# Optimization experiments

Measured on AMD Instinct MI355X. Metric: run time of the kernel, lower is better.

## Reference

```python
import jax, jax.numpy as jnp
import numpy as np

IN_NC = 32
OUT_NC = 32
HIDDEN = 192  # in_nc * expand_ratio(6)
KS = 3
EPS = 1e-5


def setup_inputs() -> dict:
    key = jax.random.key(0)
    k1, k2 = jax.random.split(key)
    b, h, w = 8, 128, 128
    fh = fw = 8
    hyper = IN_NC * HIDDEN + HIDDEN * KS * KS + HIDDEN * OUT_NC  # 14016
    return {
        "x": jax.random.normal(k1, (b, IN_NC, h, w), jnp.float32),
        "s": jax.random.normal(k2, (b, hyper, fh, fw), jnp.float32),
        "g1": jnp.ones((HIDDEN,), jnp.float32),
        "b1": jnp.zeros((HIDDEN,), jnp.float32),
        "g2": jnp.ones((HIDDEN,), jnp.float32),
        "b2": jnp.zeros((HIDDEN,), jnp.float32),
        "g3": jnp.ones((OUT_NC,), jnp.float32),
        "b3": jnp.zeros((OUT_NC,), jnp.float32),
    }


def _bn(x, gamma, beta):
    # x: [P, H, W, C]; training-mode BatchNorm2d over (P, H, W) per channel
    mean = jnp.mean(x, axis=(0, 1, 2))
    var = jnp.var(x, axis=(0, 1, 2))  # biased, matches torch normalization
    return (x - mean) * jax.lax.rsqrt(var + EPS) * gamma + beta


def _relu6(x):
    return jnp.clip(x, 0.0, 6.0)


def _forward(x, s, g1, b1, g2, b2, g3, b3):
    b, c, h, w = x.shape
    fh, fw = s.shape[-2], s.shape[-1]
    ph, pw = h // fh, w // fw
    kh, kw = ph + 2, pw + 2  # padding (1,1)

    # reflect-pad then unfold into per-patch tiles [P, kh, kw, c]
    xp = jnp.pad(x, ((0, 0), (0, 0), (1, 1), (1, 1)), mode="reflect")
    xp = xp.transpose(0, 2, 3, 1)  # [b, h+2, w+2, c]
    ih = jnp.arange(fh)[:, None] * ph + jnp.arange(kh)[None, :]  # [fh, kh]
    iw = jnp.arange(fw)[:, None] * pw + jnp.arange(kw)[None, :]  # [fw, kw]
    t = xp[:, ih]            # [b, fh, kh, w+2, c]
    t = t[:, :, :, iw]       # [b, fh, kh, fw, kw, c]
    patches = t.transpose(0, 1, 3, 2, 4, 5).reshape(b * fh * fw, kh, kw, c)

    # per-patch hypernet weights
    wt = s.transpose(0, 2, 3, 1).reshape(b * fh * fw, -1)  # [P, hyper]
    r1 = IN_NC * HIDDEN
    r2 = r1 + HIDDEN * KS * KS
    w1 = wt[:, :r1].reshape(-1, HIDDEN, IN_NC)          # pointwise expand
    w2 = wt[:, r1:r2].reshape(-1, HIDDEN, KS, KS)        # depthwise 3x3
    w3 = wt[:, r2:].reshape(-1, OUT_NC, HIDDEN)          # pointwise project

    # 1x1 expand + BN + ReLU6
    x1 = jnp.einsum("pijc,poc->pijo", patches, w1)       # [P, kh, kw, hidden]
    x1 = _relu6(_bn(x1, g1, b1))

    # depthwise 3x3 (valid, stride 1) + BN + ReLU6
    ii = jnp.arange(ph)[:, None] + jnp.arange(KS)[None, :]
    jj = jnp.arange(pw)[:, None] + jnp.arange(KS)[None, :]
    win = x1[:, ii]          # [P, ph, 3, kw, hidden]
    win = win[:, :, :, jj]   # [P, ph, 3, pw, 3, hidden]
    x2 = jnp.einsum("piujvc,pcuv->pijc", win, w2)        # [P, ph, pw, hidden]
    x2 = _relu6(_bn(x2, g2, b2))

    # 1x1 project + BN
    x3 = jnp.einsum("pijc,poc->pijo", x2, w3)            # [P, ph, pw, out]
    x3 = _bn(x3, g3, b3)

    out = x3.reshape(b, fh, fw, ph, pw, OUT_NC)
    out = out.transpose(0, 5, 1, 3, 2, 4).reshape(b, OUT_NC, h, w)
    return x + out  # use_res_connect: stride==1 and in_nc==out_nc


def reference(x, s, g1, b1, g2, b2, g3, b3):
    return _forward(x, s, g1, b1, g2, b2, g3, b3)
```

## Files before the change

kernel.cpp:

```cpp
#include <hip/hip_runtime.h>

#define EPS 1e-5f

namespace {
constexpr int HYPER = 14016;
constexpr int HID   = 192;
constexpr int A1    = 324;
constexpr int A2    = 256;
constexpr int P_TOT = 512;
constexpr int W1SZ  = 6144;
constexpr int WT2SZ = 7872;
constexpr int R3OFF = 1728;

constexpr size_t WB1_B = 0;
constexpr size_t WT2_B = 6291456;
constexpr size_t X2_B  = WT2_B + 16121856;
constexpr size_t X3_B  = X2_B + 50331648;
constexpr size_t SUM_B = X3_B + 8388608;
}

typedef __attribute__((ext_vector_type(8))) short bf16x8;
typedef __attribute__((ext_vector_type(4))) float f32x4;

__device__ __forceinline__ float relu6f(float v) { return fminf(fmaxf(v, 0.f), 6.f); }

__device__ __forceinline__ float bf2f(unsigned int h) {
  return __uint_as_float(h << 16);
}
__device__ __forceinline__ unsigned short f2bf(float f) {
  unsigned int u = __float_as_uint(f);
  return (unsigned short)((u + 0x7FFFu + ((u >> 16) & 1u)) >> 16);
}

__device__ __host__ __forceinline__ int afrag_slot(int o, int c) {
  return (o >> 4) * 512 + (c >> 3) * 128 + (o & 15) * 8 + (c & 7);
}

__global__ __launch_bounds__(256) void k0_transpose(const float* __restrict__ s,
                                                    unsigned short* __restrict__ wb1,
                                                    float* __restrict__ wt2) {
  __shared__ float tile[64][65];
  const int blk = blockIdx.x;
  const int b  = blk / 219;
  const int kt = blk - b * 219;
  const int k0 = kt * 64;
  const int t  = threadIdx.x;
  {
    const int f  = t & 63;
    const int kr = t >> 6;
    const float* sp = s + ((size_t)b * HYPER + k0 + kr) * 64 + f;
#pragma unroll
    for (int kk = 0; kk < 16; kk++)
      tile[kr + kk * 4][f] = sp[(size_t)kk * 4 * 64];
  }
  __syncthreads();
  {
    const int kk = t & 63;
    const int fr = t >> 6;
    if (kt < 96) {
      const int k = k0 + kk;
      const int o = k >> 5, c = k & 31;
      const int slot = afrag_slot(o, c);
      unsigned short* wp = wb1 + ((size_t)b * 64 + fr) * W1SZ + slot;
#pragma unroll
      for (int ff = 0; ff < 16; ff++)
        wp[(size_t)ff * 4 * W1SZ] = f2bf(tile[kk][fr + ff * 4]);
    } else {
      float* wp = wt2 + ((size_t)b * 64 + fr) * WT2SZ + (k0 - W1SZ) + kk;
#pragma unroll
      for (int ff = 0; ff < 16; ff++)
        wp[(size_t)ff * 4 * WT2SZ] = tile[kk][fr + ff * 4];
    }
  }
}

__global__ __launch_bounds__(256) void k1_stats(const float* __restrict__ x,
                                                const unsigned short* __restrict__ wb1,
                                                float* __restrict__ sums) {
  __shared__ __align__(16) unsigned short pL[21 * 512];
  __shared__ float stat[384];
  const int p  = blockIdx.x;
  const int b  = p >> 6;
  const int fi = (p >> 3) & 7;
  const int fj = p & 7;
  const int t  = threadIdx.x;

  for (int i = t; i < 384; i += 256) stat[i] = 0.f;

  const int row0 = fi * 16 - 1, col0 = fj * 16 - 1;
  const float* xb = x + (size_t)b * 32 * 128 * 128;
  for (int idx = t; idx < 32 * A1; idx += 256) {
    int c  = idx / A1;
    int ij = idx - c * A1;
    int ii = ij / 18;
    int jj = ij - ii * 18;
    int r  = row0 + ii; r  = (r  < 0) ? 1 : (r  > 127) ? 126 : r;
    int cl = col0 + jj; cl = (cl < 0) ? 1 : (cl > 127) ? 126 : cl;
    int slot = ((ij >> 4) * 4 + (c >> 3)) * 128 + (ij & 15) * 8 + (c & 7);
    pL[slot] = f2bf(xb[((size_t)c * 128 + r) * 128 + cl]);
  }
  __syncthreads();

  const int lane = t & 63;
  const int wv   = t >> 6;
  const int m16  = lane & 15;
  const int quad = lane >> 4;
  const unsigned short* wbp = wb1 + (size_t)p * W1SZ;

  for (int oi = 0; oi < 3; oi++) {
    const int ot = wv + oi * 4;
    bf16x8 a = *(const bf16x8*)(wbp + ot * 512 + lane * 8);
    float sacc[4] = {0.f, 0.f, 0.f, 0.f};
    float qacc[4] = {0.f, 0.f, 0.f, 0.f};
    for (int jt = 0; jt < 21; jt++) {
      bf16x8 bb = *(const bf16x8*)&pL[jt * 512 + lane * 8];
      f32x4 d = __builtin_amdgcn_mfma_f32_16x16x32_bf16(a, bb, (f32x4){0.f, 0.f, 0.f, 0.f}, 0, 0, 0);
      const int ij = jt * 16 + m16;
      if (ij < A1) {
#pragma unroll
        for (int r = 0; r < 4; r++) {
          float v = d[r];
          sacc[r] += v;
          qacc[r] = fmaf(v, v, qacc[r]);
        }
      }
    }
#pragma unroll
    for (int r = 0; r < 4; r++) {
      float sv = sacc[r], qv = qacc[r];
#pragma unroll
      for (int msk = 1; msk < 16; msk <<= 1) {
        sv += __shfl_xor(sv, msk, 64);
        qv += __shfl_xor(qv, msk, 64);
      }
      if (m16 == 0) {
        int o = ot * 16 + quad * 4 + r;
        atomicAdd(&stat[o], sv);
        atomicAdd(&stat[192 + o], qv);
      }
    }
  }
  __syncthreads();
  for (int i = t; i < 384; i += 256) atomicAdd(&sums[i], stat[i]);
}

__global__ __launch_bounds__(256) void k2_fused(const float* __restrict__ x,
                                                const unsigned short* __restrict__ wb1,
                                                const float* __restrict__ wt2,
                                                const float* __restrict__ sums,
                                                const float* __restrict__ g1,
                                                const float* __restrict__ b1,
                                                unsigned short* __restrict__ x2,
                                                float* __restrict__ sums2) {
  __shared__ __align__(16) unsigned short pL[21 * 512];
  __shared__ __align__(16) unsigned short xc[16 * 328];
  __shared__ __align__(16) unsigned short x2s[256 * 18];
  __shared__ float w2L[HID * 9];
  __shared__ float sc[HID], sh[HID];
  __shared__ float st2[384];
  const int p  = blockIdx.x;
  const int b  = p >> 6;
  const int fi = (p >> 3) & 7;
  const int fj = p & 7;
  const int t  = threadIdx.x;

  const float inv1 = 1.f / 165888.f;
  for (int c = t; c < HID; c += 256) {
    float m   = sums[c] * inv1;
    float var = sums[192 + c] * inv1 - m * m;
    float scl = g1[c] * rsqrtf(var + EPS);
    sc[c] = scl;
    sh[c] = b1[c] - m * scl;
  }
  for (int i = t; i < 384; i += 256) st2[i] = 0.f;
  {
    const float* wtp = wt2 + (size_t)p * WT2SZ;
    for (int i = t; i < HID * 9; i += 256) w2L[i] = wtp[i];
  }

  const int row0 = fi * 16 - 1, col0 = fj * 16 - 1;
  const float* xb = x + (size_t)b * 32 * 128 * 128;
  for (int idx = t; idx < 32 * A1; idx += 256) {
    int c  = idx / A1;
    int ij = idx - c * A1;
    int ii = ij / 18;
    int jj = ij - ii * 18;
    int r  = row0 + ii; r  = (r  < 0) ? 1 : (r  > 127) ? 126 : r;
    int cl = col0 + jj; cl = (cl < 0) ? 1 : (cl > 127) ? 126 : cl;
    int slot = ((ij >> 4) * 4 + (c >> 3)) * 128 + (ij & 15) * 8 + (c & 7);
    pL[slot] = f2bf(xb[((size_t)c * 128 + r) * 128 + cl]);
  }
  __syncthreads();

  const int lane = t & 63;
  const int wv   = t >> 6;
  const int m16  = lane & 15;
  const int quad = lane >> 4;
  const int ih  = t >> 7;
  const int cdw = (t >> 3) & 15;
  const int jp  = t & 7;
  const unsigned short* wbp = wb1 + (size_t)p * W1SZ;
  unsigned short* x2base = x2 + (size_t)p * 12 * 4096;

  auto conv1 = [&](int rt) {
    bf16x8 a = *(const bf16x8*)(wbp + rt * 512 + lane * 8);
    for (int jt = wv; jt < 21; jt += 4) {
      bf16x8 bb = *(const bf16x8*)&pL[jt * 512 + lane * 8];
      f32x4 d = __builtin_amdgcn_mfma_f32_16x16x32_bf16(a, bb, (f32x4){0.f, 0.f, 0.f, 0.f}, 0, 0, 0);
      const int ij = jt * 16 + m16;
      if (ij < A1) {
#pragma unroll
        for (int r = 0; r < 4; r++) {
          int cl = quad * 4 + r;
          int ch = rt * 16 + cl;
          float v = relu6f(fmaf(d[r], sc[ch], sh[ch]));
          xc[cl * 328 + ij] = f2bf(v);
        }
      }
    }
  };

  conv1(0);
  __syncthreads();

  for (int rt = 0; rt < 12; rt++) {
    {
      const int ch = rt * 16 + cdw;
      float wr[9];
#pragma unroll
      for (int u = 0; u < 9; u++) wr[u] = w2L[ch * 9 + u];
      float a0[8], a1[8];
#pragma unroll
      for (int i = 0; i < 8; i++) { a0[i] = 0.f; a1[i] = 0.f; }
      const unsigned short* xcc = &xc[cdw * 328];
#pragma unroll
      for (int rr = 0; rr < 10; rr++) {
        const int rg = ih * 8 + rr;
        unsigned int d0 = *(const unsigned int*)&xcc[rg * 18 + jp * 2];
        unsigned int d1 = *(const unsigned int*)&xcc[rg * 18 + jp * 2 + 2];
        float v0 = bf2f(d0 & 0xFFFFu), v1 = bf2f(d0 >> 16);
        float v2 = bf2f(d1 & 0xFFFFu), v3 = bf2f(d1 >> 16);
#pragma unroll
        for (int u = 0; u < 3; u++) {
          int il = rr - u;
          if (il >= 0 && il < 8) {
            a0[il] = fmaf(v0, wr[u * 3 + 0], fmaf(v1, wr[u * 3 + 1], fmaf(v2, wr[u * 3 + 2], a0[il])));
            a1[il] = fmaf(v1, wr[u * 3 + 0], fmaf(v2, wr[u * 3 + 1], fmaf(v3, wr[u * 3 + 2], a1[il])));
          }
        }
      }
      float ls = 0.f, lq = 0.f;
#pragma unroll
      for (int il = 0; il < 8; il++) {
        const int ig = ih * 8 + il;
        const int j0 = jp * 2;
        unsigned short h0 = f2bf(a0[il]);
        unsigned short h1 = f2bf(a1[il]);
        float r0 = bf2f(h0), r1 = bf2f(h1);
        ls += r0 + r1;
        lq = fmaf(r0, r0, fmaf(r1, r1, lq));
        x2s[(ig * 16 + j0) * 18 + cdw]     = h0;
        x2s[(ig * 16 + j0 + 1) * 18 + cdw] = h1;
      }
      ls += __shfl_xor(ls, 1, 64); lq += __shfl_xor(lq, 1, 64);
      ls += __shfl_xor(ls, 2, 64); lq += __shfl_xor(lq, 2, 64);
      ls += __shfl_xor(ls, 4, 64); lq += __shfl_xor(lq, 4, 64);
      if (jp == 0) {
        atomicAdd(&st2[ch], ls);
        atomicAdd(&st2[192 + ch], lq);
      }
    }
    __syncthreads();
    {
      unsigned short* dst = x2base + (size_t)rt * 4096;
#pragma unroll
      for (int k = 0; k < 4; k++) {
        int g  = (k * 256 + t) * 4;
        int ij = g >> 4, c0 = g & 15;
        unsigned int v0 = *(const unsigned int*)&x2s[ij * 18 + c0];
        unsigned int v1 = *(const unsigned int*)&x2s[ij * 18 + c0 + 2];
        uint2 v; v.x = v0; v.y = v1;
        *(uint2*)&dst[g] = v;
      }
    }
    if (rt < 11) conv1(rt + 1);
    __syncthreads();
  }
  for (int i = t; i < 384; i += 256) atomicAdd(&sums2[i], st2[i]);
}

__global__ __launch_bounds__(256) void k3_pw2(const unsigned short* __restrict__ x2,
                                              const float* __restrict__ wt2,
                                              const float* __restrict__ sums2,
                                              const float* __restrict__ g2,
                                              const float* __restrict__ b2,
                                              unsigned short* __restrict__ x3,
                                              float* __restrict__ sums3) {
  __shared__ __align__(16) unsigned short wA[12 * 512];
  __shared__ float sc[HID], sh[HID];
  __shared__ float st3[64];
  const int blk  = blockIdx.x;
  const int p    = blk >> 1;
  const int half = blk & 1;
  const int t    = threadIdx.x;
  const float inv = 1.f / 131072.f;
  for (int c = t; c < HID; c += 256) {
    float m   = sums2[c] * inv;
    float var = sums2[192 + c] * inv - m * m;
    float scl = g2[c] * rsqrtf(var + EPS);
    sc[c] = scl;
    sh[c] = b2[c] - m * scl;
  }
  if (t < 64) st3[t] = 0.f;
  const float* w3p = wt2 + (size_t)p * WT2SZ + R3OFF;
  for (int idx = t; idx < 32 * 48; idx += 256) {
    int o  = idx / 48;
    int c4 = idx - o * 48;
    float4 v = *(const float4*)&w3p[o * HID + c4 * 4];
    int slot = ((o >> 4) * 6 + (c4 >> 3)) * 512 + ((((c4 >> 1) & 3) * 16) + (o & 15)) * 8 + (c4 & 1) * 4;
    ushort4 u;
    u.x = f2bf(v.x); u.y = f2bf(v.y); u.z = f2bf(v.z); u.w = f2bf(v.w);
    *(ushort4*)&wA[slot] = u;
  }
  __syncthreads();
  const int lane = t & 63;
  const int wv   = t >> 6;
  const int m16  = lane & 15;
  const int kg   = lane >> 4;
  bf16x8 aF[2][6];
#pragma unroll
  for (int ot = 0; ot < 2; ot++)
#pragma unroll
    for (int ks = 0; ks < 6; ks++)
      aF[ot][ks] = *(const bf16x8*)&wA[(ot * 6 + ks) * 512 + lane * 8];
  const unsigned short* x2p = x2 + (size_t)p * 12 * 4096;
  f32x4 acc[2][2];
#pragma unroll
  for (int it = 0; it < 2; it++)
#pragma unroll
    for (int ot = 0; ot < 2; ot++)
#pragma unroll
      for (int r = 0; r < 4; r++) acc[it][ot][r] = 0.f;
#pragma unroll
  for (int it = 0; it < 2; it++) {
    const int ijt = half * 8 + wv + it * 4;
    const int ij  = ijt * 16 + m16;
    const unsigned short* brow = x2p + (size_t)(kg >> 1) * 4096 + (size_t)ij * 16 + (kg & 1) * 8;
#pragma unroll
    for (int ks = 0; ks < 6; ks++) {
      ushort4 u0 = *(const ushort4*)&brow[ks * 8192];
      ushort4 u1 = *(const ushort4*)&brow[ks * 8192 + 4];
      const float* scp = &sc[ks * 32 + kg * 8];
      const float* shp = &sh[ks * 32 + kg * 8];
      unsigned short uu[8] = {u0.x, u0.y, u0.z, u0.w, u1.x, u1.y, u1.z, u1.w};
      bf16x8 bb;
#pragma unroll
      for (int j = 0; j < 8; j++) {
        float y = relu6f(fmaf(bf2f(uu[j]), scp[j], shp[j]));
        bb[j] = (short)f2bf(y);
      }
      acc[it][0] = __builtin_amdgcn_mfma_f32_16x16x32_bf16(aF[0][ks], bb, acc[it][0], 0, 0, 0);
      acc[it][1] = __builtin_amdgcn_mfma_f32_16x16x32_bf16(aF[1][ks], bb, acc[it][1], 0, 0, 0);
    }
  }
  unsigned short* x3p = x3 + (size_t)p * 32 * A2;
  float sacc[2][4] = {{0.f}}, qacc[2][4] = {{0.f}};
#pragma unroll
  for (int it = 0; it < 2; it++) {
    const int ijt = half * 8 + wv + it * 4;
#pragma unroll
    for (int ot = 0; ot < 2; ot++) {
#pragma unroll
      for (int r = 0; r < 4; r++) {
        unsigned short h = f2bf(acc[it][ot][r]);
        float v = bf2f(h);
        x3p[(size_t)(ot * 16 + kg * 4 + r) * A2 + ijt * 16 + m16] = h;
        sacc[ot][r] += v;
        qacc[ot][r] = fmaf(v, v, qacc[ot][r]);
      }
    }
  }
#pragma unroll
  for (int ot = 0; ot < 2; ot++)
#pragma unroll
    for (int r = 0; r < 4; r++) {
      float sv = sacc[ot][r], qv = qacc[ot][r];
#pragma unroll
      for (int msk = 1; msk < 16; msk <<= 1) {
        sv += __shfl_xor(sv, msk, 64);
        qv += __shfl_xor(qv, msk, 64);
      }
      if (m16 == 0) {
        int o = ot * 16 + kg * 4 + r;
        atomicAdd(&st3[o], sv);
        atomicAdd(&st3[32 + o], qv);
      }
    }
  __syncthreads();
  if (t < 64) atomicAdd(&sums3[t], st3[t]);
}

__global__ __launch_bounds__(256) void k4_out(const float* __restrict__ x,
                                              const unsigned short* __restrict__ x3,
                                              const float* __restrict__ sums3,
                                              const float* __restrict__ g3,
                                              const float* __restrict__ b3,
                                              float* __restrict__ out) {
  const int idx4 = blockIdx.x * 256 + threadIdx.x;
  const int w4 = idx4 & 31;
  int tmp = idx4 >> 5;
  const int h = tmp & 127; tmp >>= 7;
  const int o = tmp & 31;
  const int b = tmp >> 5;
  const int fi = h >> 4, i = h & 15;
  const int fj = w4 >> 2;
  const int j0 = (w4 & 3) * 4;
  const int p   = b * 64 + fi * 8 + fj;
  const int ij0 = i * 16 + j0;
  const float inv = 1.f / 131072.f;
  float m   = sums3[o] * inv;
  float var = sums3[32 + o] * inv - m * m;
  float sv  = g3[o] * rsqrtf(var + EPS);
  float shv = b3[o] - m * sv;
  float4 xv = *(const float4*)&x[(size_t)idx4 * 4];
  ushort4 u = *(const ushort4*)&x3[((size_t)p * 32 + o) * A2 + ij0];
  float4 r;
  r.x = fmaf(bf2f(u.x), sv, shv) + xv.x;
  r.y = fmaf(bf2f(u.y), sv, shv) + xv.y;
  r.z = fmaf(bf2f(u.z), sv, shv) + xv.z;
  r.w = fmaf(bf2f(u.w), sv, shv) + xv.w;
  *(float4*)&out[(size_t)idx4 * 4] = r;
}

extern "C" void kernel_launch(void* const* d_in, const int* in_sizes, int n_in,
                              void* d_out, int out_size, void* d_ws, size_t ws_size,
                              hipStream_t stream) {
  const float* x  = (const float*)d_in[0];
  const float* s  = (const float*)d_in[1];
  const float* g1 = (const float*)d_in[2];
  const float* b1 = (const float*)d_in[3];
  const float* g2 = (const float*)d_in[4];
  const float* b2 = (const float*)d_in[5];
  const float* g3 = (const float*)d_in[6];
  const float* b3 = (const float*)d_in[7];
  char* base = (char*)d_ws;
  unsigned short* wb1  = (unsigned short*)(base + WB1_B);
  float*          wt2  = (float*)(base + WT2_B);
  unsigned short* x2   = (unsigned short*)(base + X2_B);
  unsigned short* x3   = (unsigned short*)(base + X3_B);
  float*          sums = (float*)(base + SUM_B);
  float* out = (float*)d_out;

  hipMemsetAsync(sums, 0, 832 * sizeof(float), stream);
  k0_transpose<<<8 * 219, 256, 0, stream>>>(s, wb1, wt2);
  k1_stats<<<P_TOT, 256, 0, stream>>>(x, wb1, sums);
  k2_fused<<<P_TOT, 256, 0, stream>>>(x, wb1, wt2, sums, g1, b1, x2, sums + 384);
  k3_pw2<<<1024, 256, 0, stream>>>(x2, wt2, sums + 384, g2, b2, x3, sums + 768);
  k4_out<<<4096, 256, 0, stream>>>(x, x3, sums + 768, g3, b3, out);
}
```

Measured before the change: 223.0 us.

## Split fused depthwise kernel into two half-patch blocks per patch

New measurement: 228.7 us. +2.6%, slower.

```diff
diff --git a/kernel.cpp b/kernel.cpp
--- a/kernel.cpp
+++ b/kernel.cpp
@@ -152,13 +152,18 @@
                                                 const float* __restrict__ b1,
                                                 unsigned short* __restrict__ x2,
                                                 float* __restrict__ sums2) {
-  __shared__ __align__(16) unsigned short pL[21 * 512];
-  __shared__ __align__(16) unsigned short xc[16 * 328];
-  __shared__ __align__(16) unsigned short x2s[256 * 18];
+  constexpr int NIJ = 180;
+  constexpr int NT  = 12;
+  constexpr int XCP = 184;
+  __shared__ __align__(16) unsigned short pL[NT * 512];
+  __shared__ __align__(16) unsigned short xc[16 * XCP];
+  __shared__ __align__(16) unsigned short x2s[128 * 18];
   __shared__ float w2L[HID * 9];
   __shared__ float sc[HID], sh[HID];
   __shared__ float st2[384];
-  const int p  = blockIdx.x;
+  const int blk = blockIdx.x;
+  const int p  = blk >> 1;
+  const int hh = blk & 1;
   const int b  = p >> 6;
   const int fi = (p >> 3) & 7;
   const int fj = p & 7;
@@ -178,11 +183,11 @@
     for (int i = t; i < HID * 9; i += 256) w2L[i] = wtp[i];
   }
 
-  const int row0 = fi * 16 - 1, col0 = fj * 16 - 1;
+  const int row0 = fi * 16 - 1 + hh * 8, col0 = fj * 16 - 1;
   const float* xb = x + (size_t)b * 32 * 128 * 128;
-  for (int idx = t; idx < 32 * A1; idx += 256) {
-    int c  = idx / A1;
-    int ij = idx - c * A1;
+  for (int idx = t; idx < 32 * NIJ; idx += 256) {
+    int c  = idx / NIJ;
+    int ij = idx - c * NIJ;
     int ii = ij / 18;
     int jj = ij - ii * 18;
     int r  = row0 + ii; r  = (r  < 0) ? 1 : (r  > 127) ? 126 : r;
@@ -196,25 +201,25 @@
   const int wv   = t >> 6;
   const int m16  = lane & 15;
   const int quad = lane >> 4;
-  const int ih  = t >> 7;
+  const int i2  = t >> 7;
   const int cdw = (t >> 3) & 15;
   const int jp  = t & 7;
   const unsigned short* wbp = wb1 + (size_t)p * W1SZ;
-  unsigned short* x2base = x2 + (size_t)p * 12 * 4096;
+  unsigned short* x2base = x2 + (size_t)p * 12 * 4096 + (size_t)hh * 2048;
 
   auto conv1 = [&](int rt) {
     bf16x8 a = *(const bf16x8*)(wbp + rt * 512 + lane * 8);
-    for (int jt = wv; jt < 21; jt += 4) {
+    for (int jt = wv; jt < NT; jt += 4) {
       bf16x8 bb = *(const bf16x8*)&pL[jt * 512 + lane * 8];
       f32x4 d = __builtin_amdgcn_mfma_f32_16x16x32_bf16(a, bb, (f32x4){0.f, 0.f, 0.f, 0.f}, 0, 0, 0);
       const int ij = jt * 16 + m16;
-      if (ij < A1) {
+      if (ij < NIJ) {
 #pragma unroll
         for (int r = 0; r < 4; r++) {
           int cl = quad * 4 + r;
           int ch = rt * 16 + cl;
           float v = relu6f(fmaf(d[r], sc[ch], sh[ch]));
-          xc[cl * 328 + ij] = f2bf(v);
+          xc[cl * XCP + ij] = f2bf(v);
         }
       }
     }
@@ -229,13 +234,13 @@
       float wr[9];
 #pragma unroll
       for (int u = 0; u < 9; u++) wr[u] = w2L[ch * 9 + u];
-      float a0[8], a1[8];
-#pragma unroll
-      for (int i = 0; i < 8; i++) { a0[i] = 0.f; a1[i] = 0.f; }
-      const unsigned short* xcc = &xc[cdw * 328];
-#pragma unroll
-      for (int rr = 0; rr < 10; rr++) {
-        const int rg = ih * 8 + rr;
+      float a0[4], a1[4];
+#pragma unroll
+      for (int i = 0; i < 4; i++) { a0[i] = 0.f; a1[i] = 0.f; }
+      const unsigned short* xcc = &xc[cdw * XCP];
+#pragma unroll
+      for (int rr = 0; rr < 6; rr++) {
+        const int rg = i2 * 4 + rr;
         unsigned int d0 = *(const unsigned int*)&xcc[rg * 18 + jp * 2];
         unsigned int d1 = *(const unsigned int*)&xcc[rg * 18 + jp * 2 + 2];
         float v0 = bf2f(d0 & 0xFFFFu), v1 = bf2f(d0 >> 16);
@@ -243,7 +248,7 @@
 #pragma unroll
         for (int u = 0; u < 3; u++) {
           int il = rr - u;
-          if (il >= 0 && il < 8) {
+          if (il >= 0 && il < 4) {
             a0[il] = fmaf(v0, wr[u * 3 + 0], fmaf(v1, wr[u * 3 + 1], fmaf(v2, wr[u * 3 + 2], a0[il])));
             a1[il] = fmaf(v1, wr[u * 3 + 0], fmaf(v2, wr[u * 3 + 1], fmaf(v3, wr[u * 3 + 2], a1[il])));
           }
@@ -251,8 +256,8 @@
       }
       float ls = 0.f, lq = 0.f;
 #pragma unroll
-      for (int il = 0; il < 8; il++) {
-        const int ig = ih * 8 + il;
+      for (int il = 0; il < 4; il++) {
+        const int ig = i2 * 4 + il;
         const int j0 = jp * 2;
         unsigned short h0 = f2bf(a0[il]);
         unsigned short h1 = f2bf(a1[il]);
@@ -274,7 +279,7 @@
     {
       unsigned short* dst = x2base + (size_t)rt * 4096;
 #pragma unroll
-      for (int k = 0; k < 4; k++) {
+      for (int k = 0; k < 2; k++) {
         int g  = (k * 256 + t) * 4;
         int ij = g >> 4, c0 = g & 15;
         unsigned int v0 = *(const unsigned int*)&x2s[ij * 18 + c0];
@@ -454,7 +459,7 @@
   hipMemsetAsync(sums, 0, 832 * sizeof(float), stream);
   k0_transpose<<<8 * 219, 256, 0, stream>>>(s, wb1, wt2);
   k1_stats<<<P_TOT, 256, 0, stream>>>(x, wb1, sums);
-  k2_fused<<<P_TOT, 256, 0, stream>>>(x, wb1, wt2, sums, g1, b1, x2, sums + 384);
+  k2_fused<<<P_TOT * 2, 256, 0, stream>>>(x, wb1, wt2, sums, g1, b1, x2, sums + 384);
   k3_pw2<<<1024, 256, 0, stream>>>(x2, wt2, sums + 384, g2, b2, x3, sums + 768);
   k4_out<<<4096, 256, 0, stream>>>(x, x3, sums + 768, g3, b3, out);
 }
```

## Double k2 block size to 512 threads and use packed bf16 conversion instructions

Applied to the files above, without the earlier changes.

New measurement: 213.7 us. -4.2%, faster.

```diff
diff --git a/kernel.cpp b/kernel.cpp
--- a/kernel.cpp
+++ b/kernel.cpp
@@ -21,6 +21,7 @@
 
 typedef __attribute__((ext_vector_type(8))) short bf16x8;
 typedef __attribute__((ext_vector_type(4))) float f32x4;
+typedef __attribute__((ext_vector_type(4))) unsigned int u32x4;
 
 __device__ __forceinline__ float relu6f(float v) { return fminf(fmaxf(v, 0.f), 6.f); }
 
@@ -144,14 +145,14 @@
   for (int i = t; i < 384; i += 256) atomicAdd(&sums[i], stat[i]);
 }
 
-__global__ __launch_bounds__(256) void k2_fused(const float* __restrict__ x,
-                                                const unsigned short* __restrict__ wb1,
-                                                const float* __restrict__ wt2,
-                                                const float* __restrict__ sums,
-                                                const float* __restrict__ g1,
-                                                const float* __restrict__ b1,
-                                                unsigned short* __restrict__ x2,
-                                                float* __restrict__ sums2) {
+__global__ __launch_bounds__(512, 4) void k2_fused(const float* __restrict__ x,
+                                                   const unsigned short* __restrict__ wb1,
+                                                   const float* __restrict__ wt2,
+                                                   const float* __restrict__ sums,
+                                                   const float* __restrict__ g1,
+                                                   const float* __restrict__ b1,
+                                                   unsigned short* __restrict__ x2,
+                                                   float* __restrict__ sums2) {
   __shared__ __align__(16) unsigned short pL[21 * 512];
   __shared__ __align__(16) unsigned short xc[16 * 328];
   __shared__ __align__(16) unsigned short x2s[256 * 18];
@@ -165,22 +166,22 @@
   const int t  = threadIdx.x;
 
   const float inv1 = 1.f / 165888.f;
-  for (int c = t; c < HID; c += 256) {
-    float m   = sums[c] * inv1;
-    float var = sums[192 + c] * inv1 - m * m;
-    float scl = g1[c] * rsqrtf(var + EPS);
-    sc[c] = scl;
-    sh[c] = b1[c] - m * scl;
-  }
-  for (int i = t; i < 384; i += 256) st2[i] = 0.f;
+  if (t < HID) {
+    float m   = sums[t] * inv1;
+    float var = sums[192 + t] * inv1 - m * m;
+    float scl = g1[t] * rsqrtf(var + EPS);
+    sc[t] = scl;
+    sh[t] = b1[t] - m * scl;
+  }
+  if (t < 384) st2[t] = 0.f;
   {
     const float* wtp = wt2 + (size_t)p * WT2SZ;
-    for (int i = t; i < HID * 9; i += 256) w2L[i] = wtp[i];
+    for (int i = t; i < HID * 9; i += 512) w2L[i] = wtp[i];
   }
 
   const int row0 = fi * 16 - 1, col0 = fj * 16 - 1;
   const float* xb = x + (size_t)b * 32 * 128 * 128;
-  for (int idx = t; idx < 32 * A1; idx += 256) {
+  for (int idx = t; idx < 32 * A1; idx += 512) {
     int c  = idx / A1;
     int ij = idx - c * A1;
     int ii = ij / 18;
@@ -196,25 +197,31 @@
   const int wv   = t >> 6;
   const int m16  = lane & 15;
   const int quad = lane >> 4;
-  const int ih  = t >> 7;
+  const int ihq = t >> 7;
   const int cdw = (t >> 3) & 15;
   const int jp  = t & 7;
   const unsigned short* wbp = wb1 + (size_t)p * W1SZ;
-  unsigned short* x2base = x2 + (size_t)p * 12 * 4096;
+  unsigned short* x2base = x2 + (size_t)p * 49152;
 
   auto conv1 = [&](int rt) {
     bf16x8 a = *(const bf16x8*)(wbp + rt * 512 + lane * 8);
-    for (int jt = wv; jt < 21; jt += 4) {
+    float scv[4], shv[4];
+#pragma unroll
+    for (int r = 0; r < 4; r++) {
+      scv[r] = sc[rt * 16 + quad * 4 + r];
+      shv[r] = sh[rt * 16 + quad * 4 + r];
+    }
+    for (int jt = wv; jt < 21; jt += 8) {
       bf16x8 bb = *(const bf16x8*)&pL[jt * 512 + lane * 8];
       f32x4 d = __builtin_amdgcn_mfma_f32_16x16x32_bf16(a, bb, (f32x4){0.f, 0.f, 0.f, 0.f}, 0, 0, 0);
       const int ij = jt * 16 + m16;
       if (ij < A1) {
 #pragma unroll
         for (int r = 0; r < 4; r++) {
-          int cl = quad * 4 + r;
-          int ch = rt * 16 + cl;
-          float v = relu6f(fmaf(d[r], sc[ch], sh[ch]));
-          xc[cl * 328 + ij] = f2bf(v);
+          float v = relu6f(fmaf(d[r], scv[r], shv[r]));
+          unsigned int u;
+          asm("v_cvt_pk_bf16_f32 %0, %1, %2" : "=v"(u) : "v"(v), "v"(v));
+          xc[(quad * 4 + r) * 328 + ij] = (unsigned short)u;
         }
       }
     }
@@ -229,13 +236,13 @@
       float wr[9];
 #pragma unroll
       for (int u = 0; u < 9; u++) wr[u] = w2L[ch * 9 + u];
-      float a0[8], a1[8];
-#pragma unroll
-      for (int i = 0; i < 8; i++) { a0[i] = 0.f; a1[i] = 0.f; }
+      float a0[4], a1[4];
+#pragma unroll
+      for (int i = 0; i < 4; i++) { a0[i] = 0.f; a1[i] = 0.f; }
       const unsigned short* xcc = &xc[cdw * 328];
 #pragma unroll
-      for (int rr = 0; rr < 10; rr++) {
-        const int rg = ih * 8 + rr;
+      for (int rr = 0; rr < 6; rr++) {
+        const int rg = ihq * 4 + rr;
         unsigned int d0 = *(const unsigned int*)&xcc[rg * 18 + jp * 2];
         unsigned int d1 = *(const unsigned int*)&xcc[rg * 18 + jp * 2 + 2];
         float v0 = bf2f(d0 & 0xFFFFu), v1 = bf2f(d0 >> 16);
@@ -243,7 +250,7 @@
 #pragma unroll
         for (int u = 0; u < 3; u++) {
           int il = rr - u;
-          if (il >= 0 && il < 8) {
+          if (il >= 0 && il < 4) {
             a0[il] = fmaf(v0, wr[u * 3 + 0], fmaf(v1, wr[u * 3 + 1], fmaf(v2, wr[u * 3 + 2], a0[il])));
             a1[il] = fmaf(v1, wr[u * 3 + 0], fmaf(v2, wr[u * 3 + 1], fmaf(v3, wr[u * 3 + 2], a1[il])));
           }
@@ -251,16 +258,17 @@
       }
       float ls = 0.f, lq = 0.f;
 #pragma unroll
-      for (int il = 0; il < 8; il++) {
-        const int ig = ih * 8 + il;
+      for (int il = 0; il < 4; il++) {
+        const int ig = ihq * 4 + il;
         const int j0 = jp * 2;
-        unsigned short h0 = f2bf(a0[il]);
-        unsigned short h1 = f2bf(a1[il]);
-        float r0 = bf2f(h0), r1 = bf2f(h1);
-        ls += r0 + r1;
-        lq = fmaf(r0, r0, fmaf(r1, r1, lq));
-        x2s[(ig * 16 + j0) * 18 + cdw]     = h0;
-        x2s[(ig * 16 + j0 + 1) * 18 + cdw] = h1;
+        unsigned int ua;
+        asm("v_cvt_pk_bf16_f32 %0, %1, %2" : "=v"(ua) : "v"(a0[il]), "v"(a1[il]));
+        float s0 = __uint_as_float(ua << 16);
+        float s1 = __uint_as_float(ua & 0xFFFF0000u);
+        ls += s0 + s1;
+        lq = fmaf(s0, s0, fmaf(s1, s1, lq));
+        x2s[(ig * 16 + j0) * 18 + cdw]     = (unsigned short)ua;
+        x2s[(ig * 16 + j0 + 1) * 18 + cdw] = (unsigned short)(ua >> 16);
       }
       ls += __shfl_xor(ls, 1, 64); lq += __shfl_xor(lq, 1, 64);
       ls += __shfl_xor(ls, 2, 64); lq += __shfl_xor(lq, 2, 64);
@@ -274,8 +282,8 @@
     {
       unsigned short* dst = x2base + (size_t)rt * 4096;
 #pragma unroll
-      for (int k = 0; k < 4; k++) {
-        int g  = (k * 256 + t) * 4;
+      for (int k = 0; k < 2; k++) {
+        int g  = (k * 512 + t) * 4;
         int ij = g >> 4, c0 = g & 15;
         unsigned int v0 = *(const unsigned int*)&x2s[ij * 18 + c0];
         unsigned int v1 = *(const unsigned int*)&x2s[ij * 18 + c0 + 2];
@@ -286,7 +294,7 @@
     if (rt < 11) conv1(rt + 1);
     __syncthreads();
   }
-  for (int i = t; i < 384; i += 256) atomicAdd(&sums2[i], st2[i]);
+  for (int i = t; i < 384; i += 512) atomicAdd(&sums2[i], st2[i]);
 }
 
 __global__ __launch_bounds__(256) void k3_pw2(const unsigned short* __restrict__ x2,
@@ -348,17 +356,19 @@
     const unsigned short* brow = x2p + (size_t)(kg >> 1) * 4096 + (size_t)ij * 16 + (kg & 1) * 8;
 #pragma unroll
     for (int ks = 0; ks < 6; ks++) {
-      ushort4 u0 = *(const ushort4*)&brow[ks * 8192];
-      ushort4 u1 = *(const ushort4*)&brow[ks * 8192 + 4];
+      u32x4 uv = *(const u32x4*)&brow[ks * 8192];
       const float* scp = &sc[ks * 32 + kg * 8];
       const float* shp = &sh[ks * 32 + kg * 8];
-      unsigned short uu[8] = {u0.x, u0.y, u0.z, u0.w, u1.x, u1.y, u1.z, u1.w};
-      bf16x8 bb;
-#pragma unroll
-      for (int j = 0; j < 8; j++) {
-        float y = relu6f(fmaf(bf2f(uu[j]), scp[j], shp[j]));
-        bb[j] = (short)f2bf(y);
-      }
+      u32x4 pk;
+#pragma unroll
+      for (int q = 0; q < 4; q++) {
+        float ylo = relu6f(fmaf(__uint_as_float(uv[q] << 16),          scp[2 * q],     shp[2 * q]));
+        float yhi = relu6f(fmaf(__uint_as_float(uv[q] & 0xFFFF0000u),  scp[2 * q + 1], shp[2 * q + 1]));
+        unsigned int r;
+        asm("v_cvt_pk_bf16_f32 %0, %1, %2" : "=v"(r) : "v"(ylo), "v"(yhi));
+        pk[q] = r;
+      }
+      bf16x8 bb = __builtin_bit_cast(bf16x8, pk);
       acc[it][0] = __builtin_amdgcn_mfma_f32_16x16x32_bf16(aF[0][ks], bb, acc[it][0], 0, 0, 0);
       acc[it][1] = __builtin_amdgcn_mfma_f32_16x16x32_bf16(aF[1][ks], bb, acc[it][1], 0, 0, 0);
     }
@@ -371,12 +381,18 @@
 #pragma unroll
     for (int ot = 0; ot < 2; ot++) {
 #pragma unroll
-      for (int r = 0; r < 4; r++) {
-        unsigned short h = f2bf(acc[it][ot][r]);
-        float v = bf2f(h);
-        x3p[(size_t)(ot * 16 + kg * 4 + r) * A2 + ijt * 16 + m16] = h;
-        sacc[ot][r] += v;
-        qacc[ot][r] = fmaf(v, v, qacc[ot][r]);
+      for (int rp = 0; rp < 2; rp++) {
+        unsigned int ua;
+        asm("v_cvt_pk_bf16_f32 %0, %1, %2" : "=v"(ua)
+            : "v"(acc[it][ot][2 * rp]), "v"(acc[it][ot][2 * rp + 1]));
+        float v0 = __uint_as_float(ua << 16);
+        float v1 = __uint_as_float(ua & 0xFFFF0000u);
+        x3p[(size_t)(ot * 16 + kg * 4 + 2 * rp) * A2 + ijt * 16 + m16]     = (unsigned short)ua;
+        x3p[(size_t)(ot * 16 + kg * 4 + 2 * rp + 1) * A2 + ijt * 16 + m16] = (unsigned short)(ua >> 16);
+        sacc[ot][2 * rp]     += v0;
+        sacc[ot][2 * rp + 1] += v1;
+        qacc[ot][2 * rp]      = fmaf(v0, v0, qacc[ot][2 * rp]);
+        qacc[ot][2 * rp + 1]  = fmaf(v1, v1, qacc[ot][2 * rp + 1]);
       }
     }
   }
@@ -454,7 +470,7 @@
   hipMemsetAsync(sums, 0, 832 * sizeof(float), stream);
   k0_transpose<<<8 * 219, 256, 0, stream>>>(s, wb1, wt2);
   k1_stats<<<P_TOT, 256, 0, stream>>>(x, wb1, sums);
-  k2_fused<<<P_TOT, 256, 0, stream>>>(x, wb1, wt2, sums, g1, b1, x2, sums + 384);
+  k2_fused<<<P_TOT, 512, 0, stream>>>(x, wb1, wt2, sums, g1, b1, x2, sums + 384);
   k3_pw2<<<1024, 256, 0, stream>>>(x2, wt2, sums + 384, g2, b2, x3, sums + 768);
   k4_out<<<4096, 256, 0, stream>>>(x, x3, sums + 768, g3, b3, out);
 }
```
